# Kernel tuning notes

Hardware: AMD Instinct MI355X
Metric: run time of the kernel (lower is better)

Reference implementation:

```python
import jax, jax.numpy as jnp
from jax import lax
import numpy as np


def box15(x, axis):
    # sliding sum of 15 consecutive elements along axis (same math as the
    # cumsum trick in the original find_nn)
    cs = jnp.cumsum(x, axis=axis)
    first = lax.slice_in_dim(cs, 14, 15, axis=axis)
    rest = lax.slice_in_dim(cs, 15, cs.shape[axis], axis=axis) - \
           lax.slice_in_dim(cs, 0, cs.shape[axis] - 15, axis=axis)
    return jnp.concatenate([first, rest], axis=axis)


def find_nn_sorted(seq):
    # seq: (b,3,f,h,w). Returns sorted 14-NN patch indices (b,1,f-6,h-88,w-88,14)
    b, c, f, h, w = seq.shape
    Hd, Wd = h - 74, w - 74
    gh, gw = h - 88, w - 88
    seq_n = seq[:, :, 3:f - 3, 37:h - 37, 37:w - 37]
    base = jnp.arange(b * f * (h - 14) * (w - 14), dtype=jnp.int32).reshape(b, f, h - 14, w - 14)
    base = base[:, 3:f - 3, 37:h - 51, 37:w - 51].reshape(-1)  # (P,)
    P = base.shape[0]
    hs = jnp.arange(75)

    def dist_one(ts, vs, hv):
        win = lax.dynamic_slice(seq, (0, 0, ts, vs, hv), (b, c, f - 6, Hd, Wd))
        d = jnp.mean((win - seq_n) ** 2, axis=1)           # (b,f-6,Hd,Wd)
        return box15(box15(d, -1), -2).reshape(-1)          # (P,)

    def step(carry, tv):
        dmin, imin = carry                                  # (P,14) each
        ts, vs = tv // 75, tv % 75
        dists = jax.vmap(lambda hv: dist_one(ts, vs, hv))(hs)   # (75,P)
        self_mask = (ts == 3) & (vs == 37)
        dists = jnp.where(self_mask & (hs == 37)[:, None], jnp.inf, dists)
        off = ((ts - 3) * (h - 14) * (w - 14) + (vs - 37) * (w - 14) + (hs - 37)).astype(jnp.int32)
        cand_i = base[None, :] + off[:, None]               # (75,P)
        cat_d = jnp.concatenate([dmin, dists.T], axis=1)    # (P,89)
        cat_i = jnp.concatenate([imin, cand_i.T], axis=1)
        negd, pos = lax.top_k(-cat_d, 14)                   # 14 smallest dists, ascending
        return (-negd, jnp.take_along_axis(cat_i, pos, axis=1)), None

    init = (jnp.full((P, 14), jnp.inf, seq.dtype), jnp.zeros((P, 14), jnp.int32))
    (dmin, imin), _ = lax.scan(step, init, jnp.arange(7 * 75))
    return imin.reshape(b, 1, f - 6, gh, gw, 14)


def create_layers(seq_c, min_i):
    # seq_c: (b,3,f,h2,w2); min_i: (b,1,f-6,h2-80,w2-80,14)
    b, c, f, h2, w2 = seq_c.shape
    H6, W6 = h2 - 6, w2 - 6
    self_i = jnp.arange(b * f * H6 * W6, dtype=jnp.int32).reshape(b, 1, f, H6, W6)
    self_i = self_i[:, :, 3:f - 3, 37:H6 - 37, 37:W6 - 37][..., None]
    mi = jnp.concatenate([self_i, min_i], axis=-1)          # (b,1,1,Hg,Wg,15)
    mi = jnp.moveaxis(mi[:, 0, 0], -1, 1)                   # (b,15,Hg,Wg)
    sp = jnp.transpose(seq_c, (0, 2, 3, 4, 1))              # (b,f,h2,w2,3)
    r = jnp.arange(7)
    out = jnp.zeros((b, 15, 49, 3, h2 - 74, w2 - 74), seq_c.dtype)
    for mv in range(7):
        Kv = (h2 - 74 - mv) // 7
        for mh in range(7):
            Kh = (w2 - 74 - mh) // 7
            sel = mi[:, :, mv:mv + 7 * Kv:7, mh:mh + 7 * Kh:7]   # (b,15,Kv,Kh)
            bi = sel // (f * H6 * W6); rem = sel % (f * H6 * W6)
            fi = rem // (H6 * W6); rem = rem % (H6 * W6)
            pv = rem // W6; ph = rem % W6
            patch = sp[bi[..., None, None], fi[..., None, None],
                       pv[..., None, None] + r[:, None],
                       ph[..., None, None] + r[None, :], :]      # (b,15,Kv,Kh,7,7,3)
            img = patch.transpose(0, 1, 6, 2, 4, 3, 5).reshape(b, 15, 3, 7 * Kv, 7 * Kh)
            out = out.at[:, :, mv * 7 + mh, :, mv:mv + 7 * Kv, mh:mh + 7 * Kh].set(img)
    out = out[..., 6:-6, 6:-6]
    return out.reshape(b, 15, 147, h2 - 86, w2 - 86)


def refl3(x):
    return jnp.pad(x, ((0, 0), (0, 0), (3, 3), (3, 3)), mode='reflect')


def sep_fm(x, w_vh, w_f, w_n):
    # SepConvFM2D: grouped 7x7 spatial conv, grouped 1x1 feature conv, grouped 1x1 neighbor conv
    b, n, fch, v, h = x.shape
    n_out = w_n.shape[0] // fch
    y = refl3(x.reshape(b, n * fch, v, h))
    y = lax.conv_general_dilated(y, w_vh, (1, 1), 'VALID', feature_group_count=(fch // 3) * n)
    y = lax.conv_general_dilated(y, w_f, (1, 1), 'VALID', feature_group_count=n)
    y = y.reshape(b, n, fch, v, h).transpose(0, 2, 1, 3, 4).reshape(b, fch * n, v, h)
    y = lax.conv_general_dilated(y, w_n, (1, 1), 'VALID', feature_group_count=fch)
    return y.reshape(b, fch, n_out, v, h).transpose(0, 2, 1, 3, 4)


def bn_train(x, g, be):
    m = x.mean(axis=(0, 2, 3), keepdims=True)
    v = jnp.mean((x - m) ** 2, axis=(0, 2, 3), keepdims=True)
    return g[None, :, None, None] * (x - m) / jnp.sqrt(v + 1e-5) + be[None, :, None, None]


def sep_conv_net(x, params):
    (w_vh0, w_f0, w_n0, b0, w_vh1, w_f1, w_n1, g1, be1, w_vh2, w_f2, w_n2, g2, be2,
     w_vh3, w_f3, w_n3, g3, be3, w_vh4, w_f4, b4) = params
    x = jax.nn.relu(sep_fm(x, w_vh0, w_f0, w_n0) + b0)
    for (wv, wf, wn, g, be) in ((w_vh1, w_f1, w_n1, g1, be1),
                                (w_vh2, w_f2, w_n2, g2, be2),
                                (w_vh3, w_f3, w_n3, g3, be3)):
        x = sep_fm(x, wv, wf, wn)
        b_, n, fch, v, h = x.shape
        x = bn_train(x.reshape(b_, n * fch, v, h), g, be).reshape(b_, n, fch, v, h)
        x = jax.nn.relu(x)
    y = refl3(x[:, 0])                                       # (b,150,v,h)
    y = lax.conv_general_dilated(y, w_vh4, (1, 1), 'VALID', feature_group_count=50)
    y = lax.conv_general_dilated(y, w_f4, (1, 1), 'VALID')
    return y + b4


def vid_cnn(seq_in, params):
    min_i = find_nn_sorted(lax.stop_gradient(seq_in))        # indices are non-differentiable
    seq_c = seq_in[..., 4:-4, 4:-4]
    layers = create_layers(seq_c, min_i)                     # (b,15,147,V,W)
    valid = seq_c[:, :, 3:-3, 43:-43, 43:-43][:, :, 0]       # (b,3,V,W)
    wts = (layers - layers[:, 0:1]) ** 2
    b, n, _, v, h = wts.shape
    wts = wts.reshape(b, n, 49, 3, v, h).mean(axis=2)
    x_f = jnp.concatenate([layers, wts], axis=2)             # (b,15,150,V,W)
    return valid - sep_conv_net(x_f, params)


def setup_inputs() -> dict:
    key = jax.random.key(0)
    ks = jax.random.split(key, 32)
    def nrm(k, shape, s=0.05):
        return (jax.random.normal(k, shape) * s).astype(jnp.float32)
    inp = {'seq_in': jax.random.normal(ks[0], (1, 3, 7, 160, 160), jnp.float32),
           'gpu_usage': 0}
    pairs = [(15, 8), (8, 4), (4, 2), (2, 1)]
    ki = 1
    for l, (ni, no) in enumerate(pairs):
        inp['w_vh%d' % l] = nrm(ks[ki], (150 * ni, 3, 7, 7)); ki += 1
        inp['w_f%d' % l] = nrm(ks[ki], (150 * ni, 150, 1, 1)); ki += 1
        inp['w_n%d' % l] = nrm(ks[ki], (150 * no, ni, 1, 1)); ki += 1
    inp['b0'] = nrm(ks[ki], (1, 8, 150, 1, 1)); ki += 1
    for l, (ni, no) in enumerate(pairs):
        if l == 0:
            continue
        inp['g%d' % l] = (1.0 + nrm(ks[ki], (150 * no,), 0.02)).astype(jnp.float32); ki += 1
        inp['be%d' % l] = nrm(ks[ki], (150 * no,), 0.02); ki += 1
    inp['w_vh4'] = nrm(ks[ki], (150, 3, 7, 7)); ki += 1
    inp['w_f4'] = nrm(ks[ki], (3, 150, 1, 1)); ki += 1
    inp['b4'] = nrm(ks[ki], (1, 3, 1, 1)); ki += 1
    return inp


def reference(seq_in, w_vh0, w_f0, w_n0, b0, w_vh1, w_f1, w_n1, g1, be1,
              w_vh2, w_f2, w_n2, g2, be2, w_vh3, w_f3, w_n3, g3, be3,
              w_vh4, w_f4, b4, gpu_usage):
    params = (w_vh0, w_f0, w_n0, b0, w_vh1, w_f1, w_n1, g1, be1,
              w_vh2, w_f2, w_n2, g2, be2, w_vh3, w_f3, w_n3, g3, be3,
              w_vh4, w_f4, b4)
    return vid_cnn(seq_in, params)
```

## Files before the change

### kernel.cpp

```cpp
#include <hip/hip_runtime.h>
#include <cstdint>
#include <cstddef>

#define H160   160
#define HD     86
#define GW     72
#define PG     5184
#define P66    4356
#define NPAIR  2178
#define IDX146 21316
#define NVNH   5625
#define SELF_CAND 19687
#define CHUNK  2625
#define NCHUNK 15
#define NSLOT  21
#define SLOTLEN 125
typedef unsigned long long u64;
struct F3 { float x, y, z; };

__global__ void k0_transpose(const float* __restrict__ seq, float* __restrict__ seqT3) {
  int t7 = blockIdx.y;
  int x  = blockIdx.x;
  int y  = threadIdx.x;
  int o = ((t7 * H160 + x) * H160 + y) * 3;
  seqT3[o + 0] = seq[(0 * 7 + t7) * 25600 + y * H160 + x];
  seqT3[o + 1] = seq[(1 * 7 + t7) * 25600 + y * H160 + x];
  seqT3[o + 2] = seq[(2 * 7 + t7) * 25600 + y * H160 + x];
}

__global__ void k_init(u64* __restrict__ sk, int n) {
  int i = blockIdx.x * 256 + threadIdx.x;
  if (i < n) sk[i] = ~0ULL;
}

__global__ __launch_bounds__(128) void k1_dist(const float* __restrict__ seqT3,
                                               float* __restrict__ wsD, int chunkBase) {
  __shared__ float cs[HD][87];
  const float R3 = 0.33333334f;
  int cand = chunkBase + (int)blockIdx.x;
  int ts = cand / NVNH;
  int rr = cand % NVNH;
  int vs = rr / 75;
  int hv = rr % 75;
  int t = threadIdx.x;
  if (t < HD) {
    const F3* pa = (const F3*)seqT3 + ((ts * H160 + hv) * H160 + (vs + t));
    const F3* pb = (const F3*)seqT3 + ((3  * H160 + 37) * H160 + (37 + t));
    float c0 = 0.f;
    int x = 0;
#pragma unroll 1
    for (int blk = 0; blk < 10; ++blk) {
      F3 Av[8], Bv[8];
#pragma unroll
      for (int u = 0; u < 8; ++u) { Av[u] = pa[(x + u) * H160]; Bv[u] = pb[(x + u) * H160]; }
#pragma unroll
      for (int u = 0; u < 8; ++u) {
        float d0 = __fsub_rn(Av[u].x, Bv[u].x);
        float d1 = __fsub_rn(Av[u].y, Bv[u].y);
        float d2 = __fsub_rn(Av[u].z, Bv[u].z);
        float s  = __fadd_rn(__fadd_rn(__fmul_rn(d0, d0), __fmul_rn(d1, d1)), __fmul_rn(d2, d2));
        float q0 = __fmul_rn(s, R3);
        float e  = __builtin_fmaf(-3.0f, q0, s);
        float dd = __builtin_fmaf(e, R3, q0);
        c0 = __fadd_rn(c0, dd);
        cs[t][x + u] = c0;
      }
      x += 8;
    }
    {
      F3 Av[6], Bv[6];
#pragma unroll
      for (int u = 0; u < 6; ++u) { Av[u] = pa[(80 + u) * H160]; Bv[u] = pb[(80 + u) * H160]; }
#pragma unroll
      for (int u = 0; u < 6; ++u) {
        float d0 = __fsub_rn(Av[u].x, Bv[u].x);
        float d1 = __fsub_rn(Av[u].y, Bv[u].y);
        float d2 = __fsub_rn(Av[u].z, Bv[u].z);
        float s  = __fadd_rn(__fadd_rn(__fmul_rn(d0, d0), __fmul_rn(d1, d1)), __fmul_rn(d2, d2));
        float q0 = __fmul_rn(s, R3);
        float e  = __builtin_fmaf(-3.0f, q0, s);
        float dd = __builtin_fmaf(e, R3, q0);
        c0 = __fadd_rn(c0, dd);
        cs[t][80 + u] = c0;
      }
    }
  }
  __syncthreads();
  if (t < GW) {
    int jm = (t == 0) ? 0 : (t - 1);
    float cc = 0.f;
    float ring[16];
    float* D = wsD + (size_t)blockIdx.x * PG;
#pragma unroll
    for (int r = 0; r < HD; ++r) {
      float v = (t == 0) ? cs[r][14] : __fsub_rn(cs[r][t + 14], cs[r][jm]);
      cc = __fadd_rn(cc, v);
      ring[r & 15] = cc;
      if (r >= 14) {
        int gy = r - 14;
        float out = (gy == 0) ? cc : __fsub_rn(cc, ring[(gy - 1) & 15]);
        D[gy * GW + t] = out;
      }
    }
  }
}

__global__ __launch_bounds__(256) void k2_topk(const float* __restrict__ wsD,
                                               u64* __restrict__ sk, int chunkBase) {
  __shared__ u64 lk[5][14][64];
  int tid = threadIdx.x;
  int w = tid >> 6, lane = tid & 63;
  int s = blockIdx.y;
  int pid = (int)blockIdx.x * 64 + lane;
  int st  = (w == 0) ? 96 : (w - 1) * 32;
  int cnt = (w == 0) ? 29 : 32;

  if (w == 0) {
#pragma unroll
    for (int k = 0; k < 14; ++k)
      lk[4][k][lane] = sk[(size_t)(s * 14 + k) * PG + pid];
  }
  float dv[32];
  const float* Dp = wsD + (size_t)(s * SLOTLEN + st) * PG + pid;
#pragma unroll
  for (int u = 0; u < 32; ++u)
    if (u < cnt) dv[u] = Dp[(size_t)u * PG];

  u64 key[14];
#pragma unroll
  for (int k = 0; k < 14; ++k) key[k] = ~0ULL;
  int cand0 = chunkBase + s * SLOTLEN + st;
#pragma unroll
  for (int u = 0; u < 32; ++u) {
    if (u < cnt) {
      int cand = cand0 + u;
      if (cand != SELF_CAND) {
        u64 nk = ((u64)__float_as_uint(dv[u]) << 32) | (unsigned)cand;
        if (nk < key[13]) {
#pragma unroll
          for (int j = 13; j >= 1; --j)
            key[j] = (nk < key[j - 1]) ? key[j - 1] : ((nk < key[j]) ? nk : key[j]);
          if (nk < key[0]) key[0] = nk;
        }
      }
    }
  }
#pragma unroll
  for (int k = 0; k < 14; ++k) lk[w][k][lane] = key[k];
  __syncthreads();
  if (w != 0) return;

  int h0 = 0, h1 = 0, h2 = 0, h3 = 0, h4 = 0;
  u64 a0 = lk[0][0][lane], a1 = lk[1][0][lane], a2 = lk[2][0][lane],
      a3 = lk[3][0][lane], a4 = lk[4][0][lane];
#pragma unroll
  for (int o = 0; o < 14; ++o) {
    u64 b01 = a0 < a1 ? a0 : a1; int j01 = a0 < a1 ? 0 : 1;
    u64 b23 = a2 < a3 ? a2 : a3; int j23 = a2 < a3 ? 2 : 3;
    u64 b03 = b01 < b23 ? b01 : b23; int j03 = b01 < b23 ? j01 : j23;
    u64 best = b03 < a4 ? b03 : a4; int bj = b03 < a4 ? j03 : 4;
    sk[(size_t)(s * 14 + o) * PG + pid] = best;
    h0 += (bj == 0); h1 += (bj == 1); h2 += (bj == 2); h3 += (bj == 3); h4 += (bj == 4);
    int c0 = h0 < 14 ? h0 : 13, c1 = h1 < 14 ? h1 : 13, c2 = h2 < 14 ? h2 : 13,
        c3 = h3 < 14 ? h3 : 13, c4 = h4 < 14 ? h4 : 13;
    a0 = lk[0][c0][lane]; if (h0 >= 14) a0 = ~0ULL;
    a1 = lk[1][c1][lane]; if (h1 >= 14) a1 = ~0ULL;
    a2 = lk[2][c2][lane]; if (h2 >= 14) a2 = ~0ULL;
    a3 = lk[3][c3][lane]; if (h3 >= 14) a3 = ~0ULL;
    a4 = lk[4][c4][lane]; if (h4 >= 14) a4 = ~0ULL;
  }
}

__global__ __launch_bounds__(64) void k_merge(const u64* __restrict__ sk,
                                              int* __restrict__ fsi) {
  int pid = (int)blockIdx.x * 64 + threadIdx.x;
  int gy = pid / GW, gx = pid % GW;
  int cur[NSLOT];
#pragma unroll
  for (int s = 0; s < NSLOT; ++s) cur[s] = 0;
  for (int o = 0; o < 14; ++o) {
    u64 bk = ~0ULL; int bs = 0;
#pragma unroll
    for (int s = 0; s < NSLOT; ++s) {
      int cc = cur[s] < 14 ? cur[s] : 13;
      u64 kk = sk[(size_t)(s * 14 + cc) * PG + pid];
      if (cur[s] >= 14) kk = ~0ULL;
      if (kk < bk) { bk = kk; bs = s; }
    }
#pragma unroll
    for (int s = 0; s < NSLOT; ++s) cur[s] += (bs == s) ? 1 : 0;
    int cand = (int)(unsigned)(bk & 0xffffffffULL);
    int ts = cand / NVNH;
    int rr = cand % NVNH;
    int vs = rr / 75, hv = rr % 75;
    fsi[o * PG + pid] = ts * IDX146 + (gy + vs) * 146 + (gx + hv);
  }
}

__global__ void k3_layers(const float* __restrict__ seq, const int* __restrict__ fsi,
                          float* __restrict__ X) {
  int n = blockIdx.y;
  int p = (int)blockIdx.x * 256 + threadIdx.x;
  if (p >= P66) return;
  int yo = p / 66, xo = p % 66;
  int y = yo + 6, x = xo + 6;
  float sv0 = seq[(0 * 7 + 3) * 25600 + (41 + y) * H160 + (41 + x)];
  float sv1 = seq[(1 * 7 + 3) * 25600 + (41 + y) * H160 + (41 + x)];
  float sv2 = seq[(2 * 7 + 3) * 25600 + (41 + y) * H160 + (41 + x)];
  float w0 = 0.f, w1 = 0.f, w2 = 0.f;
  for (int mv = 0; mv < 7; ++mv) {
    int dy = (y - mv) % 7; int gyy = y - dy;
    for (int mh = 0; mh < 7; ++mh) {
      int dx = (x - mh) % 7; int gxx = x - dx;
      int q = mv * 7 + mh;
      float v0, v1, v2;
      if (n == 0) { v0 = sv0; v1 = sv1; v2 = sv2; }
      else {
        int idx = fsi[(n - 1) * PG + gyy * GW + gxx];
        int fi = idx / IDX146; int rem = idx % IDX146;
        int pv = rem / 146, ph = rem % 146;
        int base = (4 + pv + dy) * H160 + (4 + ph + dx);
        v0 = seq[(0 * 7 + fi) * 25600 + base];
        v1 = seq[(1 * 7 + fi) * 25600 + base];
        v2 = seq[(2 * 7 + fi) * 25600 + base];
      }
      X[(size_t)(n * 150 + q * 3 + 0) * P66 + p] = v0;
      X[(size_t)(n * 150 + q * 3 + 1) * P66 + p] = v1;
      X[(size_t)(n * 150 + q * 3 + 2) * P66 + p] = v2;
      float e0 = v0 - sv0, e1 = v1 - sv1, e2 = v2 - sv2;
      w0 += e0 * e0; w1 += e1 * e1; w2 += e2 * e2;
    }
  }
  X[(size_t)(n * 150 + 147) * P66 + p] = w0 / 49.f;
  X[(size_t)(n * 150 + 148) * P66 + p] = w1 / 49.f;
  X[(size_t)(n * 150 + 149) * P66 + p] = w2 / 49.f;
}

__global__ void k4a_vh(const float* __restrict__ in, const float* __restrict__ w,
                       float* __restrict__ out) {
  int g = blockIdx.y;
  int p = (int)blockIdx.x * 256 + threadIdx.x;
  if (p >= P66) return;
  int yo = p / 66, xo = p % 66;
  int o0 = g * 3;
  int iyt[7], ixt[7];
#pragma unroll
  for (int k = 0; k < 7; ++k) {
    int vy = yo + k - 3; iyt[k] = (vy < 0 ? -vy : (vy > 65 ? 130 - vy : vy)) * 66;
    int vx = xo + k - 3; ixt[k] = vx < 0 ? -vx : (vx > 65 ? 130 - vx : vx);
  }
  float a0 = 0.f, a1 = 0.f, a2 = 0.f;
#pragma unroll
  for (int ic = 0; ic < 3; ++ic) {
    const float* ip = in + (size_t)(o0 + ic) * P66;
    const float* wp = w + (size_t)o0 * 147 + ic * 49;
#pragma unroll
    for (int ky = 0; ky < 7; ++ky) {
      const float* row = ip + iyt[ky];
#pragma unroll
      for (int kx = 0; kx < 7; ++kx) {
        float v = row[ixt[kx]];
        int wi = ky * 7 + kx;
        a0 = fmaf(v, wp[wi],       a0);
        a1 = fmaf(v, wp[147 + wi], a1);
        a2 = fmaf(v, wp[294 + wi], a2);
      }
    }
  }
  out[(size_t)(o0 + 0) * P66 + p] = a0;
  out[(size_t)(o0 + 1) * P66 + p] = a1;
  out[(size_t)(o0 + 2) * P66 + p] = a2;
}

__global__ void k4b_f(const float* __restrict__ in, const float* __restrict__ w,
                      float* __restrict__ out) {
  int ob = blockIdx.y * 10;
  int p = (int)blockIdx.x * 256 + threadIdx.x;
  if (p >= P66) return;
  int gb = (ob / 150) * 150;
  float acc[10];
#pragma unroll
  for (int j = 0; j < 10; ++j) acc[j] = 0.f;
  const float* ip = in + (size_t)gb * P66 + p;
  const float* w0 = w + (size_t)ob * 150;
  for (int f = 0; f < 150; ++f) {
    float v = ip[(size_t)f * P66];
#pragma unroll
    for (int j = 0; j < 10; ++j) acc[j] = fmaf(v, w0[j * 150 + f], acc[j]);
  }
#pragma unroll
  for (int j = 0; j < 10; ++j) out[(size_t)(ob + j) * P66 + p] = acc[j];
}

template<int NI, int NO>
__global__ void k4c_n(const float* __restrict__ in, const float* __restrict__ w,
                      const float* __restrict__ bias, float* __restrict__ out, int withbias) {
  int f = blockIdx.y;
  int q = (int)blockIdx.x * 256 + threadIdx.x;
  if (q >= NPAIR) return;
  int p = q * 2;
  float2 acc[NO];
#pragma unroll
  for (int j = 0; j < NO; ++j) { acc[j].x = 0.f; acc[j].y = 0.f; }
#pragma unroll
  for (int nn = 0; nn < NI; ++nn) {
    float2 v = *(const float2*)&in[(size_t)(nn * 150 + f) * P66 + p];
#pragma unroll
    for (int j = 0; j < NO; ++j) {
      float wv = w[(f * NO + j) * NI + nn];
      acc[j].x = fmaf(v.x, wv, acc[j].x);
      acc[j].y = fmaf(v.y, wv, acc[j].y);
    }
  }
#pragma unroll
  for (int j = 0; j < NO; ++j) {
    float2 r = acc[j];
    if (withbias) {
      float b = bias[j * 150 + f];
      r.x += b; r.x = r.x > 0.f ? r.x : 0.f;
      r.y += b; r.y = r.y > 0.f ? r.y : 0.f;
    }
    *(float2*)&out[(size_t)(j * 150 + f) * P66 + p] = r;
  }
}

__global__ void k_bn(float* __restrict__ x, const float* __restrict__ g,
                     const float* __restrict__ be) {
  int c = blockIdx.x;
  float* xp = x + (size_t)c * P66;
  __shared__ float red[256];
  int t = threadIdx.x;
  float s = 0.f;
  for (int p = t; p < P66; p += 256) s += xp[p];
  red[t] = s; __syncthreads();
  for (int off = 128; off > 0; off >>= 1) { if (t < off) red[t] += red[t + off]; __syncthreads(); }
  float m = red[0] / (float)P66;
  __syncthreads();
  float s2 = 0.f;
  for (int p = t; p < P66; p += 256) { float dd = xp[p] - m; s2 += dd * dd; }
  red[t] = s2; __syncthreads();
  for (int off = 128; off > 0; off >>= 1) { if (t < off) red[t] += red[t + off]; __syncthreads(); }
  float var = red[0] / (float)P66;
  float sc = g[c] / sqrtf(var + 1e-5f);
  float sh = be[c] - m * sc;
  for (int p = t; p < P66; p += 256) { float r = fmaf(xp[p], sc, sh); xp[p] = r > 0.f ? r : 0.f; }
}

__global__ void k_final(const float* __restrict__ in, const float* __restrict__ wf,
                        const float* __restrict__ b4, const float* __restrict__ seq,
                        float* __restrict__ out) {
  int p = (int)blockIdx.x * 256 + threadIdx.x;
  if (p >= P66) return;
  int yo = p / 66, xo = p % 66;
  float a0 = 0.f, a1 = 0.f, a2 = 0.f;
  for (int f = 0; f < 150; ++f) {
    float v = in[(size_t)f * P66 + p];
    a0 = fmaf(v, wf[f],       a0);
    a1 = fmaf(v, wf[150 + f], a1);
    a2 = fmaf(v, wf[300 + f], a2);
  }
  float y0 = a0 + b4[0], y1 = a1 + b4[1], y2 = a2 + b4[2];
  int vo = (47 + yo) * H160 + (47 + xo);
  out[0 * P66 + p] = seq[(0 * 7 + 3) * 25600 + vo] - y0;
  out[1 * P66 + p] = seq[(1 * 7 + 3) * 25600 + vo] - y1;
  out[2 * P66 + p] = seq[(2 * 7 + 3) * 25600 + vo] - y2;
}

extern "C" void kernel_launch(void* const* d_in, const int* in_sizes, int n_in,
                              void* d_out, int out_size, void* d_ws, size_t ws_size,
                              hipStream_t stream) {
  const float* seq   = (const float*)d_in[0];
  const float* w_vh0 = (const float*)d_in[2];
  const float* w_f0  = (const float*)d_in[3];
  const float* w_n0  = (const float*)d_in[4];
  const float* w_vh1 = (const float*)d_in[5];
  const float* w_f1  = (const float*)d_in[6];
  const float* w_n1  = (const float*)d_in[7];
  const float* w_vh2 = (const float*)d_in[8];
  const float* w_f2  = (const float*)d_in[9];
  const float* w_n2  = (const float*)d_in[10];
  const float* w_vh3 = (const float*)d_in[11];
  const float* w_f3  = (const float*)d_in[12];
  const float* w_n3  = (const float*)d_in[13];
  const float* b0    = (const float*)d_in[14];
  const float* g1    = (const float*)d_in[15];
  const float* be1   = (const float*)d_in[16];
  const float* g2    = (const float*)d_in[17];
  const float* be2   = (const float*)d_in[18];
  const float* g3    = (const float*)d_in[19];
  const float* be3   = (const float*)d_in[20];
  const float* w_vh4 = (const float*)d_in[21];
  const float* w_f4  = (const float*)d_in[22];
  const float* b4    = (const float*)d_in[23];
  float* outp = (float*)d_out;

  float* fws   = (float*)d_ws;
  float* seqT3 = fws;
  u64*   sk    = (u64*)(seqT3 + 537600);
  float* X     = (float*)(sk + 1524096);
  float* A     = X + 9801000;
  int*   fsi   = (int*)(A + 9801000);
  float* wsD   = X;

  k0_transpose<<<dim3(160, 7), 160, 0, stream>>>(seq, seqT3);
  k_init<<<(1524096 + 255) / 256, 256, 0, stream>>>(sk, 1524096);
  for (int c = 0; c < NCHUNK; ++c) {
    k1_dist<<<CHUNK, 128, 0, stream>>>(seqT3, wsD, c * CHUNK);
    k2_topk<<<dim3(81, NSLOT), 256, 0, stream>>>(wsD, sk, c * CHUNK);
  }
  k_merge<<<81, 64, 0, stream>>>(sk, fsi);
  k3_layers<<<dim3(18, 15), 256, 0, stream>>>(seq, fsi, X);

  k4a_vh<<<dim3(18, 750), 256, 0, stream>>>(X, w_vh0, A);
  k4b_f <<<dim3(18, 225), 256, 0, stream>>>(A, w_f0, X);
  k4c_n<15, 8><<<dim3(9, 150), 256, 0, stream>>>(X, w_n0, b0, A, 1);
  k4a_vh<<<dim3(18, 400), 256, 0, stream>>>(A, w_vh1, X);
  k4b_f <<<dim3(18, 120), 256, 0, stream>>>(X, w_f1, A);
  k4c_n<8, 4><<<dim3(9, 150), 256, 0, stream>>>(A, w_n1, nullptr, X, 0);
  k_bn<<<600, 256, 0, stream>>>(X, g1, be1);
  k4a_vh<<<dim3(18, 200), 256, 0, stream>>>(X, w_vh2, A);
  k4b_f <<<dim3(18, 60), 256, 0, stream>>>(A, w_f2, X);
  k4c_n<4, 2><<<dim3(9, 150), 256, 0, stream>>>(X, w_n2, nullptr, A, 0);
  k_bn<<<300, 256, 0, stream>>>(A, g2, be2);
  k4a_vh<<<dim3(18, 100), 256, 0, stream>>>(A, w_vh3, X);
  k4b_f <<<dim3(18, 30), 256, 0, stream>>>(X, w_f3, A);
  k4c_n<2, 1><<<dim3(9, 150), 256, 0, stream>>>(A, w_n3, nullptr, X, 0);
  k_bn<<<150, 256, 0, stream>>>(X, g3, be3);
  k4a_vh<<<dim3(18, 50), 256, 0, stream>>>(X, w_vh4, A);
  k_final<<<18, 256, 0, stream>>>(A, w_f4, b4, seq, outp);
}
```

Baseline: 1.959 ms.

## Process three adjacent candidates per block in distance kernel, widen 1x1 conv tile

The distance kernel now handles three consecutive horizontal-offset candidates per block. Each loaded window row is reused for three shifted reference rows held in registers, and the first box filter is applied in registers with ring buffers instead of storing prefix sums to shared memory. The vertical box pass is spread over 216 tasks across two rounds. Separately, the 1x1 conv kernel computes 15 output channels per thread instead of 10, with grid sizes adjusted to match. This cuts global loads and block count, but raises register pressure and relies on CHUNK (2625) being divisible by 3 so that each triple of candidates shares the same ts/vs row.

```diff
diff --git a/kernel.cpp b/kernel.cpp
--- a/kernel.cpp
+++ b/kernel.cpp
@@ -35,71 +35,109 @@
 
 __global__ __launch_bounds__(128) void k1_dist(const float* __restrict__ seqT3,
                                                float* __restrict__ wsD, int chunkBase) {
-  __shared__ float cs[HD][87];
+  __shared__ float v[3][HD][73];
   const float R3 = 0.33333334f;
-  int cand = chunkBase + (int)blockIdx.x;
-  int ts = cand / NVNH;
-  int rr = cand % NVNH;
+  int cand0 = chunkBase + (int)blockIdx.x * 3;
+  int ts = cand0 / NVNH;
+  int rr = cand0 % NVNH;
   int vs = rr / 75;
-  int hv = rr % 75;
+  int hv0 = rr % 75;
   int t = threadIdx.x;
   if (t < HD) {
-    const F3* pa = (const F3*)seqT3 + ((ts * H160 + hv) * H160 + (vs + t));
+    const F3* pa = (const F3*)seqT3 + ((ts * H160 + hv0) * H160 + (vs + t));
     const F3* pb = (const F3*)seqT3 + ((3  * H160 + 37) * H160 + (37 + t));
-    float c0 = 0.f;
-    int x = 0;
+    float c0 = 0.f, c1 = 0.f, c2 = 0.f;
+    float r0[16], r1[16], r2[16];
+    F3 pb0, pb1, pb2;
 #pragma unroll 1
-    for (int blk = 0; blk < 10; ++blk) {
-      F3 Av[8], Bv[8];
-#pragma unroll
-      for (int u = 0; u < 8; ++u) { Av[u] = pa[(x + u) * H160]; Bv[u] = pb[(x + u) * H160]; }
-#pragma unroll
-      for (int u = 0; u < 8; ++u) {
-        float d0 = __fsub_rn(Av[u].x, Bv[u].x);
-        float d1 = __fsub_rn(Av[u].y, Bv[u].y);
-        float d2 = __fsub_rn(Av[u].z, Bv[u].z);
-        float s  = __fadd_rn(__fadd_rn(__fmul_rn(d0, d0), __fmul_rn(d1, d1)), __fmul_rn(d2, d2));
-        float q0 = __fmul_rn(s, R3);
-        float e  = __builtin_fmaf(-3.0f, q0, s);
-        float dd = __builtin_fmaf(e, R3, q0);
-        c0 = __fadd_rn(c0, dd);
-        cs[t][x + u] = c0;
+    for (int blk = 0; blk < 6; ++blk) {
+#pragma unroll
+      for (int k = 0; k < 16; ++k) {
+        int u = blk * 16 + k;
+        if (u < 88) {
+          F3 A = pa[u * H160];
+          pb2 = pb1; pb1 = pb0;
+          if (u < 86) pb0 = pb[u * H160];
+          if (u < 86) {
+            float d0 = __fsub_rn(A.x, pb0.x);
+            float d1 = __fsub_rn(A.y, pb0.y);
+            float d2 = __fsub_rn(A.z, pb0.z);
+            float s  = __fadd_rn(__fadd_rn(__fmul_rn(d0, d0), __fmul_rn(d1, d1)), __fmul_rn(d2, d2));
+            float q0 = __fmul_rn(s, R3);
+            float e  = __builtin_fmaf(-3.0f, q0, s);
+            float dd = __builtin_fmaf(e, R3, q0);
+            c0 = __fadd_rn(c0, dd);
+            r0[u & 15] = c0;
+            if (u >= 14) {
+              int j = u - 14;
+              v[0][t][j] = (j == 0) ? c0 : __fsub_rn(c0, r0[(k + 1) & 15]);
+            }
+          }
+          {
+            int xq = u - 1;
+            if (xq >= 0 && xq < 86) {
+              float d0 = __fsub_rn(A.x, pb1.x);
+              float d1 = __fsub_rn(A.y, pb1.y);
+              float d2 = __fsub_rn(A.z, pb1.z);
+              float s  = __fadd_rn(__fadd_rn(__fmul_rn(d0, d0), __fmul_rn(d1, d1)), __fmul_rn(d2, d2));
+              float q0 = __fmul_rn(s, R3);
+              float e  = __builtin_fmaf(-3.0f, q0, s);
+              float dd = __builtin_fmaf(e, R3, q0);
+              c1 = __fadd_rn(c1, dd);
+              r1[(k + 15) & 15] = c1;
+              if (xq >= 14) {
+                int j = xq - 14;
+                v[1][t][j] = (j == 0) ? c1 : __fsub_rn(c1, r1[k & 15]);
+              }
+            }
+          }
+          {
+            int xq = u - 2;
+            if (xq >= 0 && xq < 86) {
+              float d0 = __fsub_rn(A.x, pb2.x);
+              float d1 = __fsub_rn(A.y, pb2.y);
+              float d2 = __fsub_rn(A.z, pb2.z);
+              float s  = __fadd_rn(__fadd_rn(__fmul_rn(d0, d0), __fmul_rn(d1, d1)), __fmul_rn(d2, d2));
+              float q0 = __fmul_rn(s, R3);
+              float e  = __builtin_fmaf(-3.0f, q0, s);
+              float dd = __builtin_fmaf(e, R3, q0);
+              c2 = __fadd_rn(c2, dd);
+              r2[(k + 14) & 15] = c2;
+              if (xq >= 14) {
+                int j = xq - 14;
+                v[2][t][j] = (j == 0) ? c2 : __fsub_rn(c2, r2[(k + 15) & 15]);
+              }
+            }
+          }
+        }
       }
-      x += 8;
-    }
-    {
-      F3 Av[6], Bv[6];
-#pragma unroll
-      for (int u = 0; u < 6; ++u) { Av[u] = pa[(80 + u) * H160]; Bv[u] = pb[(80 + u) * H160]; }
-#pragma unroll
-      for (int u = 0; u < 6; ++u) {
-        float d0 = __fsub_rn(Av[u].x, Bv[u].x);
-        float d1 = __fsub_rn(Av[u].y, Bv[u].y);
-        float d2 = __fsub_rn(Av[u].z, Bv[u].z);
-        float s  = __fadd_rn(__fadd_rn(__fmul_rn(d0, d0), __fmul_rn(d1, d1)), __fmul_rn(d2, d2));
-        float q0 = __fmul_rn(s, R3);
-        float e  = __builtin_fmaf(-3.0f, q0, s);
-        float dd = __builtin_fmaf(e, R3, q0);
-        c0 = __fadd_rn(c0, dd);
-        cs[t][80 + u] = c0;
-      }
     }
   }
   __syncthreads();
-  if (t < GW) {
-    int jm = (t == 0) ? 0 : (t - 1);
-    float cc = 0.f;
-    float ring[16];
-    float* D = wsD + (size_t)blockIdx.x * PG;
-#pragma unroll
-    for (int r = 0; r < HD; ++r) {
-      float v = (t == 0) ? cs[r][14] : __fsub_rn(cs[r][t + 14], cs[r][jm]);
-      cc = __fadd_rn(cc, v);
-      ring[r & 15] = cc;
-      if (r >= 14) {
-        int gy = r - 14;
-        float out = (gy == 0) ? cc : __fsub_rn(cc, ring[(gy - 1) & 15]);
-        D[gy * GW + t] = out;
+#pragma unroll 1
+  for (int rd = 0; rd < 2; ++rd) {
+    int task = t + rd * 128;
+    if (task < 216) {
+      int q = task / GW, cq = task % GW;
+      float cc = 0.f;
+      float ring[16];
+      float* D = wsD + (size_t)((int)blockIdx.x * 3 + q) * PG + cq;
+#pragma unroll 1
+      for (int rb = 0; rb < 6; ++rb) {
+#pragma unroll
+        for (int k = 0; k < 16; ++k) {
+          int r = rb * 16 + k;
+          if (r < HD) {
+            float val = v[q][r][cq];
+            cc = __fadd_rn(cc, val);
+            ring[k] = cc;
+            if (r >= 14) {
+              int gy = r - 14;
+              float out = (gy == 0) ? cc : __fsub_rn(cc, ring[(k + 1) & 15]);
+              D[gy * GW] = out;
+            }
+          }
+        }
       }
     }
   }
@@ -274,22 +312,22 @@
 
 __global__ void k4b_f(const float* __restrict__ in, const float* __restrict__ w,
                       float* __restrict__ out) {
-  int ob = blockIdx.y * 10;
+  int ob = blockIdx.y * 15;
   int p = (int)blockIdx.x * 256 + threadIdx.x;
   if (p >= P66) return;
   int gb = (ob / 150) * 150;
-  float acc[10];
-#pragma unroll
-  for (int j = 0; j < 10; ++j) acc[j] = 0.f;
+  float acc[15];
+#pragma unroll
+  for (int j = 0; j < 15; ++j) acc[j] = 0.f;
   const float* ip = in + (size_t)gb * P66 + p;
   const float* w0 = w + (size_t)ob * 150;
   for (int f = 0; f < 150; ++f) {
     float v = ip[(size_t)f * P66];
 #pragma unroll
-    for (int j = 0; j < 10; ++j) acc[j] = fmaf(v, w0[j * 150 + f], acc[j]);
-  }
-#pragma unroll
-  for (int j = 0; j < 10; ++j) out[(size_t)(ob + j) * P66 + p] = acc[j];
+    for (int j = 0; j < 15; ++j) acc[j] = fmaf(v, w0[j * 150 + f], acc[j]);
+  }
+#pragma unroll
+  for (int j = 0; j < 15; ++j) out[(size_t)(ob + j) * P66 + p] = acc[j];
 }
 
 template<int NI, int NO>
@@ -405,25 +443,25 @@
   k0_transpose<<<dim3(160, 7), 160, 0, stream>>>(seq, seqT3);
   k_init<<<(1524096 + 255) / 256, 256, 0, stream>>>(sk, 1524096);
   for (int c = 0; c < NCHUNK; ++c) {
-    k1_dist<<<CHUNK, 128, 0, stream>>>(seqT3, wsD, c * CHUNK);
+    k1_dist<<<CHUNK / 3, 128, 0, stream>>>(seqT3, wsD, c * CHUNK);
     k2_topk<<<dim3(81, NSLOT), 256, 0, stream>>>(wsD, sk, c * CHUNK);
   }
   k_merge<<<81, 64, 0, stream>>>(sk, fsi);
   k3_layers<<<dim3(18, 15), 256, 0, stream>>>(seq, fsi, X);
 
   k4a_vh<<<dim3(18, 750), 256, 0, stream>>>(X, w_vh0, A);
-  k4b_f <<<dim3(18, 225), 256, 0, stream>>>(A, w_f0, X);
+  k4b_f <<<dim3(18, 150), 256, 0, stream>>>(A, w_f0, X);
   k4c_n<15, 8><<<dim3(9, 150), 256, 0, stream>>>(X, w_n0, b0, A, 1);
   k4a_vh<<<dim3(18, 400), 256, 0, stream>>>(A, w_vh1, X);
-  k4b_f <<<dim3(18, 120), 256, 0, stream>>>(X, w_f1, A);
+  k4b_f <<<dim3(18, 80), 256, 0, stream>>>(X, w_f1, A);
   k4c_n<8, 4><<<dim3(9, 150), 256, 0, stream>>>(A, w_n1, nullptr, X, 0);
   k_bn<<<600, 256, 0, stream>>>(X, g1, be1);
   k4a_vh<<<dim3(18, 200), 256, 0, stream>>>(X, w_vh2, A);
-  k4b_f <<<dim3(18, 60), 256, 0, stream>>>(A, w_f2, X);
+  k4b_f <<<dim3(18, 40), 256, 0, stream>>>(A, w_f2, X);
   k4c_n<4, 2><<<dim3(9, 150), 256, 0, stream>>>(X, w_n2, nullptr, A, 0);
   k_bn<<<300, 256, 0, stream>>>(A, g2, be2);
   k4a_vh<<<dim3(18, 100), 256, 0, stream>>>(A, w_vh3, X);
-  k4b_f <<<dim3(18, 30), 256, 0, stream>>>(X, w_f3, A);
+  k4b_f <<<dim3(18, 20), 256, 0, stream>>>(X, w_f3, A);
   k4c_n<2, 1><<<dim3(9, 150), 256, 0, stream>>>(A, w_n3, nullptr, X, 0);
   k_bn<<<150, 256, 0, stream>>>(X, g3, be3);
   k4a_vh<<<dim3(18, 50), 256, 0, stream>>>(X, w_vh4, A);
```

New measurement: 2.613 ms. 33.4% more time.
